# Performance work log

Measured on AMD Instinct MI355X. Metric: run time of the kernel, lower is better.

Reference implementation:

```python
import jax, jax.numpy as jnp
import numpy as np

B, S, D_IN, D_OUT = 4, 2048, 1024, 1024


def setup_inputs() -> dict:
    key = jax.random.key(0)
    ks = jax.random.split(key, 7)
    return {
        "X": jax.random.normal(ks[0], (B, S, D_IN), dtype=jnp.float32),
        "Wq": jax.random.normal(ks[1], (D_IN, D_OUT), dtype=jnp.float32) * (1.0 / np.sqrt(D_IN)),
        "bq": jax.random.normal(ks[2], (D_OUT,), dtype=jnp.float32) * 0.02,
        "Wk": jax.random.normal(ks[3], (D_IN, D_OUT), dtype=jnp.float32) * (1.0 / np.sqrt(D_IN)),
        "bk": jax.random.normal(ks[4], (D_OUT,), dtype=jnp.float32) * 0.02,
        "Wv": jax.random.normal(ks[5], (D_IN, D_OUT), dtype=jnp.float32) * (1.0 / np.sqrt(D_IN)),
        "bv": jax.random.normal(ks[6], (D_OUT,), dtype=jnp.float32) * 0.02,
    }


def reference(X, Wq, bq, Wk, bk, Wv, bv):
    # Linear projections (torch Linear: x @ W^T + b; here W stored as [in,out])
    Q = X @ Wq + bq  # [B,S,D]
    K = X @ Wk + bk
    V = X @ Wv + bv
    dk = jnp.sqrt(jnp.asarray(D_OUT, dtype=X.dtype))
    # Raw scores, lower-triangular ZEROING (not -inf), scale, softmax over keys.
    S_ = jnp.einsum('bqd,bkd->bqk', Q, K)
    S_ = jnp.tril(S_) / dk
    A = jax.nn.softmax(S_, axis=2)  # [B,S,S]
    # Faithful to torch.einsum('ijk,ijl->ijl', A, V): reduces A over k, scales V.
    out = jnp.einsum('bqk,bql->bql', A, V)
    return out
```

## Files before the change

kernel.cpp:

```cpp
#include <hip/hip_runtime.h>
#include <hip/hip_bf16.h>

#define DIN  1024
#define DOUT 1024
#define MROWS 8192

#define BM 256
#define BN 128
#define BK 64
#define NKT (DIN / BK)

typedef __attribute__((ext_vector_type(8))) short short8;
typedef __attribute__((ext_vector_type(4))) float f32x4;

__device__ __forceinline__ ushort f2bf(float f) {
    union { float f; unsigned u; } x; x.f = f;
    unsigned u = x.u + 0x7fffu + ((x.u >> 16) & 1u);
    return (ushort)(u >> 16);
}

__global__ void prep_kernel(const float* __restrict__ X, ushort* __restrict__ Xb,
                            const float* __restrict__ W, ushort* __restrict__ Wt) {
    __shared__ float tile[32][33];
    const int b = blockIdx.x;
    if (b < 2048) {
        const float4* X4 = (const float4*)X;
        ushort4* O4 = (ushort4*)Xb;
        const int n4 = MROWS * DIN / 4;
        for (int idx = b * 256 + threadIdx.x; idx < n4; idx += 2048 * 256) {
            float4 v = X4[idx];
            ushort4 o;
            o.x = f2bf(v.x); o.y = f2bf(v.y); o.z = f2bf(v.z); o.w = f2bf(v.w);
            O4[idx] = o;
        }
    } else {
        const int t = b - 2048;
        const int bx = (t & 31) * 32;
        const int by = (t >> 5) * 32;
        const int tx = threadIdx.x & 31;
        const int ty = threadIdx.x >> 5;
#pragma unroll
        for (int i = 0; i < 32; i += 8)
            tile[ty + i][tx] = W[(size_t)(by + ty + i) * DOUT + (bx + tx)];
        __syncthreads();
#pragma unroll
        for (int i = 0; i < 32; i += 8)
            Wt[(size_t)(bx + ty + i) * DIN + (by + tx)] = f2bf(tile[tx][ty + i]);
    }
}

__global__ __launch_bounds__(512, 2) void gemm_bias(
    const ushort* __restrict__ Xb,
    const ushort* __restrict__ Wt,
    const float* __restrict__ bias,
    float* __restrict__ out)
{
    __shared__ ushort As[3][BM * BK];
    __shared__ ushort Bs[3][BN * BK];

    const int tid  = threadIdx.x;
    const int lane = tid & 63;
    const int wid  = tid >> 6;
    const int wr   = wid >> 1;
    const int wc   = wid & 1;

    const int bid = blockIdx.x;
    const int swz = (bid & 7) * 32 + (bid >> 3);
    const int bm = (swz >> 3) * BM;
    const int bn = (swz & 7) * BN;

    auto stageHalf = [&](int b, int kt, int h) {
#pragma unroll
        for (int j = 0; j < 2; ++j) {
            const int c   = j * 512 + tid;
            const int rl  = c >> 3;
            const int scc = (c & 7) ^ (rl & 7);
            __builtin_amdgcn_global_load_lds(
                (const __attribute__((address_space(1))) void*)(Xb + (size_t)(bm + h * 128 + rl) * DIN + kt * BK + scc * 8),
                (__attribute__((address_space(3))) void*)(&As[b][h * 8192 + (j * 512 + wid * 64) * 8]),
                16, 0, 0);
        }
        {
            const int c   = tid;
            const int rl  = c >> 3;
            const int scc = (c & 7) ^ (rl & 7);
            __builtin_amdgcn_global_load_lds(
                (const __attribute__((address_space(1))) void*)(Wt + (size_t)(bn + h * 64 + rl) * DIN + kt * BK + scc * 8),
                (__attribute__((address_space(3))) void*)(&Bs[b][h * 4096 + wid * 512]),
                16, 0, 0);
        }
    };

    f32x4 acc[4][4];
#pragma unroll
    for (int i = 0; i < 4; ++i)
#pragma unroll
        for (int j = 0; j < 4; ++j)
            acc[i][j] = (f32x4){0.f, 0.f, 0.f, 0.f};

    auto tileBody = [&](int buf, bool doStage, int sbuf, int skt, int wait, bool bar) {
        if (doStage) {
            stageHalf(sbuf, skt, 0);
            stageHalf(sbuf, skt, 1);
        }
        short8 af[2][4], bfr[2][4];
#pragma unroll
        for (int ks = 0; ks < 2; ++ks) {
            const int sc = ((ks * 4 + (lane >> 4)) ^ (lane & 7)) * 8;
            const int am = wr * 64 + (lane & 15);
            const int bnr = wc * 64 + (lane & 15);
#pragma unroll
            for (int i = 0; i < 4; ++i)
                af[ks][i] = *(const short8*)(&As[buf][(am + i * 16) * 64 + sc]);
#pragma unroll
            for (int j = 0; j < 4; ++j)
                bfr[ks][j] = *(const short8*)(&Bs[buf][(bnr + j * 16) * 64 + sc]);
        }
        __builtin_amdgcn_s_setprio(1);
#pragma unroll
        for (int ks = 0; ks < 2; ++ks)
#pragma unroll
            for (int i = 0; i < 4; ++i)
#pragma unroll
                for (int j = 0; j < 4; ++j)
                    acc[i][j] = __builtin_amdgcn_mfma_f32_16x16x32_bf16(af[ks][i], bfr[ks][j], acc[i][j], 0, 0, 0);
        __builtin_amdgcn_s_setprio(0);
        if (wait == 2)      asm volatile("s_waitcnt vmcnt(6) lgkmcnt(0)" ::: "memory");
        else if (wait == 1) asm volatile("s_waitcnt vmcnt(0) lgkmcnt(0)" ::: "memory");
        else                asm volatile("s_waitcnt lgkmcnt(0)" ::: "memory");
        __builtin_amdgcn_sched_barrier(0);
        if (bar) __builtin_amdgcn_s_barrier();
    };

    stageHalf(0, 0, 0);
    stageHalf(0, 0, 1);
    stageHalf(1, 1, 0);
    stageHalf(1, 1, 1);
    asm volatile("s_waitcnt vmcnt(6)" ::: "memory");
    __builtin_amdgcn_sched_barrier(0);
    __builtin_amdgcn_s_barrier();

    for (int t = 0; t < NKT - 2; ++t)
        tileBody(t % 3, true, (t + 2) % 3, t + 2, 2, true);
    tileBody((NKT - 2) % 3, false, 0, 0, 1, true);
    tileBody((NKT - 1) % 3, false, 0, 0, 0, false);

    const int crow = bm + wr * 64 + (lane >> 4) * 4;
    const int ccol = bn + wc * 64 + (lane & 15);
#pragma unroll
    for (int j = 0; j < 4; ++j) {
        const int col = ccol + j * 16;
        const float bval = bias[col];
#pragma unroll
        for (int i = 0; i < 4; ++i) {
#pragma unroll
            for (int r = 0; r < 4; ++r)
                out[(size_t)(crow + i * 16 + r) * DOUT + col] = acc[i][j][r] + bval;
        }
    }
}

__global__ void gemm_naive(const float* __restrict__ X, const float* __restrict__ W,
                           const float* __restrict__ b, float* __restrict__ out) {
    int n = blockIdx.x * blockDim.x + threadIdx.x;
    int m = blockIdx.y;
    float acc = b[n];
    for (int k = 0; k < DIN; ++k)
        acc += X[(size_t)m * DIN + k] * W[(size_t)k * DOUT + n];
    out[(size_t)m * DOUT + n] = acc;
}

extern "C" void kernel_launch(void* const* d_in, const int* in_sizes, int n_in,
                              void* d_out, int out_size, void* d_ws, size_t ws_size,
                              hipStream_t stream) {
    const float* X  = (const float*)d_in[0];
    const float* Wv = (const float*)d_in[5];
    const float* bv = (const float*)d_in[6];
    float* out = (float*)d_out;

    const size_t xb_elems = (size_t)MROWS * DIN;
    const size_t wt_elems = (size_t)DOUT * DIN;
    const size_t needed = (xb_elems + wt_elems) * sizeof(ushort);

    if (ws_size < needed) {
        dim3 g(DOUT / 256, MROWS);
        gemm_naive<<<g, 256, 0, stream>>>(X, Wv, bv, out);
        return;
    }

    ushort* Xb = (ushort*)d_ws;
    ushort* Wt = Xb + xb_elems;

    prep_kernel<<<2048 + 1024, 256, 0, stream>>>(X, Xb, Wv, Wt);
    gemm_bias<<<256, 512, 0, stream>>>(Xb, Wt, bv, out);
}
```

Before: 40.62 us.

## Fuse fp32-to-bf16 conversion of X into GEMM via register-staged A tiles

Drops the separate pass that converts X to bf16 into a workspace. The GEMM now loads fp32 X rows into registers, converts them and writes swizzled bf16 into LDS, while W^T still arrives by direct global-to-LDS DMA. This removes a full write and re-read of the bf16 copy of X. In exchange, the pipeline shrinks from a triple-buffered, partially waited schedule to a double buffer with a full vmcnt(0) wait every k-step, register pressure rises, and each block reads twice as many bytes of X.

```diff
diff --git a/kernel.cpp b/kernel.cpp
--- a/kernel.cpp
+++ b/kernel.cpp
@@ -19,44 +19,30 @@
     return (ushort)(u >> 16);
 }
 
-__global__ void prep_kernel(const float* __restrict__ X, ushort* __restrict__ Xb,
-                            const float* __restrict__ W, ushort* __restrict__ Wt) {
+__global__ void prep_wt(const float* __restrict__ W, ushort* __restrict__ Wt) {
     __shared__ float tile[32][33];
-    const int b = blockIdx.x;
-    if (b < 2048) {
-        const float4* X4 = (const float4*)X;
-        ushort4* O4 = (ushort4*)Xb;
-        const int n4 = MROWS * DIN / 4;
-        for (int idx = b * 256 + threadIdx.x; idx < n4; idx += 2048 * 256) {
-            float4 v = X4[idx];
-            ushort4 o;
-            o.x = f2bf(v.x); o.y = f2bf(v.y); o.z = f2bf(v.z); o.w = f2bf(v.w);
-            O4[idx] = o;
-        }
-    } else {
-        const int t = b - 2048;
-        const int bx = (t & 31) * 32;
-        const int by = (t >> 5) * 32;
-        const int tx = threadIdx.x & 31;
-        const int ty = threadIdx.x >> 5;
+    const int t  = blockIdx.x;
+    const int bx = (t & 31) * 32;
+    const int by = (t >> 5) * 32;
+    const int tx = threadIdx.x & 31;
+    const int ty = threadIdx.x >> 5;
 #pragma unroll
-        for (int i = 0; i < 32; i += 8)
-            tile[ty + i][tx] = W[(size_t)(by + ty + i) * DOUT + (bx + tx)];
-        __syncthreads();
+    for (int i = 0; i < 32; i += 8)
+        tile[ty + i][tx] = W[(size_t)(by + ty + i) * DOUT + (bx + tx)];
+    __syncthreads();
 #pragma unroll
-        for (int i = 0; i < 32; i += 8)
-            Wt[(size_t)(bx + ty + i) * DIN + (by + tx)] = f2bf(tile[tx][ty + i]);
-    }
+    for (int i = 0; i < 32; i += 8)
+        Wt[(size_t)(bx + ty + i) * DIN + (by + tx)] = f2bf(tile[tx][ty + i]);
 }
 
-__global__ __launch_bounds__(512, 2) void gemm_bias(
-    const ushort* __restrict__ Xb,
+__global__ __launch_bounds__(512, 2) void gemm_fused(
+    const float*  __restrict__ X,
     const ushort* __restrict__ Wt,
-    const float* __restrict__ bias,
+    const float*  __restrict__ bias,
     float* __restrict__ out)
 {
-    __shared__ ushort As[3][BM * BK];
-    __shared__ ushort Bs[3][BN * BK];
+    __shared__ ushort As[2][BM * BK];
+    __shared__ ushort Bs[2][BN * BK];
 
     const int tid  = threadIdx.x;
     const int lane = tid & 63;
@@ -69,24 +55,38 @@
     const int bm = (swz >> 3) * BM;
     const int bn = (swz & 7) * BN;
 
-    auto stageHalf = [&](int b, int kt, int h) {
+    const int ar_ = tid >> 1;
+    const int ah_ = tid & 1;
+    const float* aSrc = X + (size_t)(bm + ar_) * DIN + ah_ * 32;
+
+    float4 areg[8];
+    auto loadA = [&](int kt) {
+        const float4* p = (const float4*)(aSrc + kt * BK);
+#pragma unroll
+        for (int i = 0; i < 8; ++i) areg[i] = p[i];
+    };
+    auto writeA = [&](int b) {
+        ushort* row = &As[b][ar_ * BK];
+#pragma unroll
+        for (int w = 0; w < 4; ++w) {
+            const float4 a0 = areg[w * 2], a1 = areg[w * 2 + 1];
+            short8 v;
+            v[0] = f2bf(a0.x); v[1] = f2bf(a0.y); v[2] = f2bf(a0.z); v[3] = f2bf(a0.w);
+            v[4] = f2bf(a1.x); v[5] = f2bf(a1.y); v[6] = f2bf(a1.z); v[7] = f2bf(a1.w);
+            const int slot = (ah_ * 4 + w) ^ (ar_ & 7);
+            *(short8*)(row + slot * 8) = v;
+        }
+    };
+
+    auto dmaB = [&](int b, int kt) {
 #pragma unroll
         for (int j = 0; j < 2; ++j) {
-            const int c   = j * 512 + tid;
-            const int rl  = c >> 3;
-            const int scc = (c & 7) ^ (rl & 7);
+            const int c  = j * 512 + tid;
+            const int rl = c >> 3;
+            const int sl = (c & 7) ^ (rl & 7);
             __builtin_amdgcn_global_load_lds(
-                (const __attribute__((address_space(1))) void*)(Xb + (size_t)(bm + h * 128 + rl) * DIN + kt * BK + scc * 8),
-                (__attribute__((address_space(3))) void*)(&As[b][h * 8192 + (j * 512 + wid * 64) * 8]),
-                16, 0, 0);
-        }
-        {
-            const int c   = tid;
-            const int rl  = c >> 3;
-            const int scc = (c & 7) ^ (rl & 7);
-            __builtin_amdgcn_global_load_lds(
-                (const __attribute__((address_space(1))) void*)(Wt + (size_t)(bn + h * 64 + rl) * DIN + kt * BK + scc * 8),
-                (__attribute__((address_space(3))) void*)(&Bs[b][h * 4096 + wid * 512]),
+                (const __attribute__((address_space(1))) void*)(Wt + (size_t)(bn + rl) * DIN + kt * BK + sl * 8),
+                (__attribute__((address_space(3))) void*)(&Bs[b][(j * 512 + wid * 64) * 8]),
                 16, 0, 0);
         }
     };
@@ -98,24 +98,18 @@
         for (int j = 0; j < 4; ++j)
             acc[i][j] = (f32x4){0.f, 0.f, 0.f, 0.f};
 
-    auto tileBody = [&](int buf, bool doStage, int sbuf, int skt, int wait, bool bar) {
-        if (doStage) {
-            stageHalf(sbuf, skt, 0);
-            stageHalf(sbuf, skt, 1);
-        }
-        short8 af[2][4], bfr[2][4];
+    const int am  = wr * 64 + (lane & 15);
+    const int bnr = wc * 64 + (lane & 15);
+    auto fragRead = [&](int b, int ks, short8* af, short8* bfr) {
+        const int sc = ((ks * 4 + (lane >> 4)) ^ (lane & 7)) * 8;
 #pragma unroll
-        for (int ks = 0; ks < 2; ++ks) {
-            const int sc = ((ks * 4 + (lane >> 4)) ^ (lane & 7)) * 8;
-            const int am = wr * 64 + (lane & 15);
-            const int bnr = wc * 64 + (lane & 15);
+        for (int i = 0; i < 4; ++i)
+            af[i] = *(const short8*)(&As[b][(am + i * 16) * BK + sc]);
 #pragma unroll
-            for (int i = 0; i < 4; ++i)
-                af[ks][i] = *(const short8*)(&As[buf][(am + i * 16) * 64 + sc]);
-#pragma unroll
-            for (int j = 0; j < 4; ++j)
-                bfr[ks][j] = *(const short8*)(&Bs[buf][(bnr + j * 16) * 64 + sc]);
-        }
+        for (int j = 0; j < 4; ++j)
+            bfr[j] = *(const short8*)(&Bs[b][(bnr + j * 16) * BK + sc]);
+    };
+    auto mfmaCluster = [&](short8 af[2][4], short8 bfr[2][4]) {
         __builtin_amdgcn_s_setprio(1);
 #pragma unroll
         for (int ks = 0; ks < 2; ++ks)
@@ -125,25 +119,35 @@
                 for (int j = 0; j < 4; ++j)
                     acc[i][j] = __builtin_amdgcn_mfma_f32_16x16x32_bf16(af[ks][i], bfr[ks][j], acc[i][j], 0, 0, 0);
         __builtin_amdgcn_s_setprio(0);
-        if (wait == 2)      asm volatile("s_waitcnt vmcnt(6) lgkmcnt(0)" ::: "memory");
-        else if (wait == 1) asm volatile("s_waitcnt vmcnt(0) lgkmcnt(0)" ::: "memory");
-        else                asm volatile("s_waitcnt lgkmcnt(0)" ::: "memory");
-        __builtin_amdgcn_sched_barrier(0);
-        if (bar) __builtin_amdgcn_s_barrier();
     };
 
-    stageHalf(0, 0, 0);
-    stageHalf(0, 0, 1);
-    stageHalf(1, 1, 0);
-    stageHalf(1, 1, 1);
-    asm volatile("s_waitcnt vmcnt(6)" ::: "memory");
-    __builtin_amdgcn_sched_barrier(0);
+    loadA(0);
+    dmaB(0, 0);
+    writeA(0);
+    asm volatile("s_waitcnt vmcnt(0) lgkmcnt(0)" ::: "memory");
     __builtin_amdgcn_s_barrier();
 
-    for (int t = 0; t < NKT - 2; ++t)
-        tileBody(t % 3, true, (t + 2) % 3, t + 2, 2, true);
-    tileBody((NKT - 2) % 3, false, 0, 0, 1, true);
-    tileBody((NKT - 1) % 3, false, 0, 0, 0, false);
+    int buf = 0;
+    for (int t = 0; t < NKT - 1; ++t) {
+        loadA(t + 1);
+        dmaB(buf ^ 1, t + 1);
+        __builtin_amdgcn_sched_barrier(0);
+        short8 af[2][4], bfr[2][4];
+        fragRead(buf, 0, af[0], bfr[0]);
+        fragRead(buf, 1, af[1], bfr[1]);
+        mfmaCluster(af, bfr);
+        writeA(buf ^ 1);
+        asm volatile("s_waitcnt vmcnt(0) lgkmcnt(0)" ::: "memory");
+        __builtin_amdgcn_sched_barrier(0);
+        __builtin_amdgcn_s_barrier();
+        buf ^= 1;
+    }
+    {
+        short8 af[2][4], bfr[2][4];
+        fragRead(buf, 0, af[0], bfr[0]);
+        fragRead(buf, 1, af[1], bfr[1]);
+        mfmaCluster(af, bfr);
+    }
 
     const int crow = bm + wr * 64 + (lane >> 4) * 4;
     const int ccol = bn + wc * 64 + (lane & 15);
@@ -178,19 +182,14 @@
     const float* bv = (const float*)d_in[6];
     float* out = (float*)d_out;
 
-    const size_t xb_elems = (size_t)MROWS * DIN;
     const size_t wt_elems = (size_t)DOUT * DIN;
-    const size_t needed = (xb_elems + wt_elems) * sizeof(ushort);
-
-    if (ws_size < needed) {
+    if (ws_size < wt_elems * sizeof(ushort)) {
         dim3 g(DOUT / 256, MROWS);
         gemm_naive<<<g, 256, 0, stream>>>(X, Wv, bv, out);
         return;
     }
 
-    ushort* Xb = (ushort*)d_ws;
-    ushort* Wt = Xb + xb_elems;
-
-    prep_kernel<<<2048 + 1024, 256, 0, stream>>>(X, Xb, Wv, Wt);
-    gemm_bias<<<256, 512, 0, stream>>>(Xb, Wt, bv, out);
+    ushort* Wt = (ushort*)d_ws;
+    prep_wt<<<1024, 256, 0, stream>>>(Wv, Wt);
+    gemm_fused<<<256, 512, 0, stream>>>(X, Wt, bv, out);
 }
```

After: 62.26 us. 53.3% more time.

## Load B fragments directly from global into registers, split tile into two phases

Applied to the files above, without the earlier changes.

Removes the LDS staging buffer for the weight tile and instead has each wave load its B fragments straight from global memory into registers, double-buffered one k-tile ahead. The main loop is split into two half-k phases with a barrier and staging of A interleaved per phase, with new vmcnt thresholds. This cuts LDS traffic and capacity for B, possibly raising occupancy, but adds redundant global loads of B across waves sharing a column, more register pressure, and more barriers per tile.

```diff
diff --git a/kernel.cpp b/kernel.cpp
--- a/kernel.cpp
+++ b/kernel.cpp
@@ -56,7 +56,6 @@
     float* __restrict__ out)
 {
     __shared__ ushort As[3][BM * BK];
-    __shared__ ushort Bs[3][BN * BK];
 
     const int tid  = threadIdx.x;
     const int lane = tid & 63;
@@ -69,7 +68,7 @@
     const int bm = (swz >> 3) * BM;
     const int bn = (swz & 7) * BN;
 
-    auto stageHalf = [&](int b, int kt, int h) {
+    auto stageA = [&](int b, int kt, int h) {
 #pragma unroll
         for (int j = 0; j < 2; ++j) {
             const int c   = j * 512 + tid;
@@ -80,15 +79,15 @@
                 (__attribute__((address_space(3))) void*)(&As[b][h * 8192 + (j * 512 + wid * 64) * 8]),
                 16, 0, 0);
         }
-        {
-            const int c   = tid;
-            const int rl  = c >> 3;
-            const int scc = (c & 7) ^ (rl & 7);
-            __builtin_amdgcn_global_load_lds(
-                (const __attribute__((address_space(1))) void*)(Wt + (size_t)(bn + h * 64 + rl) * DIN + kt * BK + scc * 8),
-                (__attribute__((address_space(3))) void*)(&Bs[b][h * 4096 + wid * 512]),
-                16, 0, 0);
-        }
+    };
+
+    const ushort* bBase = Wt + (size_t)(bn + wc * 64 + (lane & 15)) * DIN + (lane >> 4) * 8;
+    auto loadB = [&](short8 (&dst)[2][4], int kt) {
+#pragma unroll
+        for (int ks = 0; ks < 2; ++ks)
+#pragma unroll
+            for (int j = 0; j < 4; ++j)
+                dst[ks][j] = *(const short8*)(bBase + (size_t)j * 16 * DIN + kt * BK + ks * 32);
     };
 
     f32x4 acc[4][4];
@@ -98,52 +97,62 @@
         for (int j = 0; j < 4; ++j)
             acc[i][j] = (f32x4){0.f, 0.f, 0.f, 0.f};
 
-    auto tileBody = [&](int buf, bool doStage, int sbuf, int skt, int wait, bool bar) {
-        if (doStage) {
-            stageHalf(sbuf, skt, 0);
-            stageHalf(sbuf, skt, 1);
-        }
-        short8 af[2][4], bfr[2][4];
-#pragma unroll
-        for (int ks = 0; ks < 2; ++ks) {
-            const int sc = ((ks * 4 + (lane >> 4)) ^ (lane & 7)) * 8;
-            const int am = wr * 64 + (lane & 15);
-            const int bnr = wc * 64 + (lane & 15);
+    const int am = wr * 64 + (lane & 15);
+
+    auto phase = [&](int buf, int ks, const short8 (&bcur)[2][4],
+                     bool doStage, int sbuf, int skt, int wait, bool endBar) {
+        short8 af[4];
+        const int sc = ((ks * 4 + (lane >> 4)) ^ (lane & 7)) * 8;
+#pragma unroll
+        for (int i = 0; i < 4; ++i)
+            af[i] = *(const short8*)(&As[buf][(am + i * 16) * BK + sc]);
+        if (doStage) stageA(sbuf, skt, ks);
+        __builtin_amdgcn_s_barrier();
+        asm volatile("s_waitcnt lgkmcnt(0)" ::: "memory");
+        __builtin_amdgcn_sched_barrier(0);
+        __builtin_amdgcn_s_setprio(1);
+        if (ks == 0) {
 #pragma unroll
             for (int i = 0; i < 4; ++i)
-                af[ks][i] = *(const short8*)(&As[buf][(am + i * 16) * 64 + sc]);
-#pragma unroll
-            for (int j = 0; j < 4; ++j)
-                bfr[ks][j] = *(const short8*)(&Bs[buf][(bnr + j * 16) * 64 + sc]);
-        }
-        __builtin_amdgcn_s_setprio(1);
-#pragma unroll
-        for (int ks = 0; ks < 2; ++ks)
+#pragma unroll
+                for (int j = 0; j < 4; ++j)
+                    acc[i][j] = __builtin_amdgcn_mfma_f32_16x16x32_bf16(af[i], bcur[0][j], acc[i][j], 0, 0, 0);
+        } else {
 #pragma unroll
             for (int i = 0; i < 4; ++i)
 #pragma unroll
                 for (int j = 0; j < 4; ++j)
-                    acc[i][j] = __builtin_amdgcn_mfma_f32_16x16x32_bf16(af[ks][i], bfr[ks][j], acc[i][j], 0, 0, 0);
+                    acc[i][j] = __builtin_amdgcn_mfma_f32_16x16x32_bf16(af[i], bcur[1][j], acc[i][j], 0, 0, 0);
+        }
         __builtin_amdgcn_s_setprio(0);
-        if (wait == 2)      asm volatile("s_waitcnt vmcnt(6) lgkmcnt(0)" ::: "memory");
-        else if (wait == 1) asm volatile("s_waitcnt vmcnt(0) lgkmcnt(0)" ::: "memory");
-        else                asm volatile("s_waitcnt lgkmcnt(0)" ::: "memory");
-        __builtin_amdgcn_sched_barrier(0);
-        if (bar) __builtin_amdgcn_s_barrier();
-    };
-
-    stageHalf(0, 0, 0);
-    stageHalf(0, 0, 1);
-    stageHalf(1, 1, 0);
-    stageHalf(1, 1, 1);
-    asm volatile("s_waitcnt vmcnt(6)" ::: "memory");
-    __builtin_amdgcn_sched_barrier(0);
+        if (wait == 12)     asm volatile("s_waitcnt vmcnt(12)" ::: "memory");
+        else if (wait == 8) asm volatile("s_waitcnt vmcnt(8)"  ::: "memory");
+        else if (wait == 0) asm volatile("s_waitcnt vmcnt(0)"  ::: "memory");
+        if (endBar) __builtin_amdgcn_s_barrier();
+    };
+
+    short8 bA[2][4], bB[2][4];
+
+    stageA(0, 0, 0); stageA(0, 0, 1);
+    loadB(bA, 0);
+    stageA(1, 1, 0); stageA(1, 1, 1);
+    asm volatile("s_waitcnt vmcnt(12)" ::: "memory");
     __builtin_amdgcn_s_barrier();
 
-    for (int t = 0; t < NKT - 2; ++t)
-        tileBody(t % 3, true, (t + 2) % 3, t + 2, 2, true);
-    tileBody((NKT - 2) % 3, false, 0, 0, 1, true);
-    tileBody((NKT - 1) % 3, false, 0, 0, 0, false);
+    auto tileBody = [&](int t, const short8 (&cur)[2][4], short8 (&nxt)[2][4],
+                        bool doLoadB, bool doStage, int wait, bool last) {
+        const int buf = t % 3;
+        if (doLoadB) loadB(nxt, t + 1);
+        phase(buf, 0, cur, doStage, (t + 2) % 3, t + 2, -1, true);
+        phase(buf, 1, cur, doStage, (t + 2) % 3, t + 2, wait, !last);
+    };
+
+    for (int tt = 0; tt < NKT - 2; tt += 2) {
+        tileBody(tt,     bA, bB, true, true, 12, false);
+        tileBody(tt + 1, bB, bA, true, true, 12, false);
+    }
+    tileBody(NKT - 2, bA, bB, true,  false, 8, false);
+    tileBody(NKT - 1, bB, bA, false, false, -1, true);
 
     const int crow = bm + wr * 64 + (lane >> 4) * 4;
     const int ccol = bn + wc * 64 + (lane & 15);
```

After: 59.43 us. +46.3%, slower.

## Shrink GEMM tile to 128x128 with simple double-buffered pipeline

Applied to the files above, without the earlier changes.

Halves the M tile to 128 rows, uses 256-thread blocks and 512 workgroups, and replaces the triple-buffered pipeline (explicit waitcnt, setprio, sched barriers) with a plain double-buffered loop synced by __syncthreads. The goal is more workgroups across the CUs and lower LDS use per block. In exchange, B-tile reuse per block drops and the hand-tuned overlap of loads and MFMA is lost.

```diff
diff --git a/kernel.cpp b/kernel.cpp
--- a/kernel.cpp
+++ b/kernel.cpp
@@ -5,7 +5,7 @@
 #define DOUT 1024
 #define MROWS 8192
 
-#define BM 256
+#define BM 128
 #define BN 128
 #define BK 64
 #define NKT (DIN / BK)
@@ -49,14 +49,14 @@
     }
 }
 
-__global__ __launch_bounds__(512, 2) void gemm_bias(
+__global__ __launch_bounds__(256, 2) void gemm_bias(
     const ushort* __restrict__ Xb,
     const ushort* __restrict__ Wt,
     const float* __restrict__ bias,
     float* __restrict__ out)
 {
-    __shared__ ushort As[3][BM * BK];
-    __shared__ ushort Bs[3][BN * BK];
+    __shared__ ushort As[2][BM * BK];
+    __shared__ ushort Bs[2][BN * BK];
 
     const int tid  = threadIdx.x;
     const int lane = tid & 63;
@@ -65,28 +65,29 @@
     const int wc   = wid & 1;
 
     const int bid = blockIdx.x;
-    const int swz = (bid & 7) * 32 + (bid >> 3);
+    const int swz = (bid & 7) * 64 + (bid >> 3);
     const int bm = (swz >> 3) * BM;
     const int bn = (swz & 7) * BN;
 
-    auto stageHalf = [&](int b, int kt, int h) {
+    auto stage = [&](int b, int kt) {
 #pragma unroll
-        for (int j = 0; j < 2; ++j) {
-            const int c   = j * 512 + tid;
+        for (int i = 0; i < 4; ++i) {
+            const int c   = i * 256 + tid;
             const int rl  = c >> 3;
             const int scc = (c & 7) ^ (rl & 7);
             __builtin_amdgcn_global_load_lds(
-                (const __attribute__((address_space(1))) void*)(Xb + (size_t)(bm + h * 128 + rl) * DIN + kt * BK + scc * 8),
-                (__attribute__((address_space(3))) void*)(&As[b][h * 8192 + (j * 512 + wid * 64) * 8]),
+                (const __attribute__((address_space(1))) void*)(Xb + (size_t)(bm + rl) * DIN + kt * BK + scc * 8),
+                (__attribute__((address_space(3))) void*)(&As[b][(i * 256 + wid * 64) * 8]),
                 16, 0, 0);
         }
-        {
-            const int c   = tid;
+#pragma unroll
+        for (int i = 0; i < 4; ++i) {
+            const int c   = i * 256 + tid;
             const int rl  = c >> 3;
             const int scc = (c & 7) ^ (rl & 7);
             __builtin_amdgcn_global_load_lds(
-                (const __attribute__((address_space(1))) void*)(Wt + (size_t)(bn + h * 64 + rl) * DIN + kt * BK + scc * 8),
-                (__attribute__((address_space(3))) void*)(&Bs[b][h * 4096 + wid * 512]),
+                (const __attribute__((address_space(1))) void*)(Wt + (size_t)(bn + rl) * DIN + kt * BK + scc * 8),
+                (__attribute__((address_space(3))) void*)(&Bs[b][(i * 256 + wid * 64) * 8]),
                 16, 0, 0);
         }
     };
@@ -98,52 +99,33 @@
         for (int j = 0; j < 4; ++j)
             acc[i][j] = (f32x4){0.f, 0.f, 0.f, 0.f};
 
-    auto tileBody = [&](int buf, bool doStage, int sbuf, int skt, int wait, bool bar) {
-        if (doStage) {
-            stageHalf(sbuf, skt, 0);
-            stageHalf(sbuf, skt, 1);
-        }
-        short8 af[2][4], bfr[2][4];
+    const int am  = wr * 64 + (lane & 15);
+    const int bnr = wc * 64 + (lane & 15);
+
+    stage(0, 0);
+    __syncthreads();
+
+    for (int t = 0; t < NKT; ++t) {
+        const int buf = t & 1;
+        if (t < NKT - 1) stage(buf ^ 1, t + 1);
 #pragma unroll
         for (int ks = 0; ks < 2; ++ks) {
+            short8 af[4], bfr[4];
             const int sc = ((ks * 4 + (lane >> 4)) ^ (lane & 7)) * 8;
-            const int am = wr * 64 + (lane & 15);
-            const int bnr = wc * 64 + (lane & 15);
 #pragma unroll
             for (int i = 0; i < 4; ++i)
-                af[ks][i] = *(const short8*)(&As[buf][(am + i * 16) * 64 + sc]);
+                af[i] = *(const short8*)(&As[buf][(am + i * 16) * BK + sc]);
 #pragma unroll
             for (int j = 0; j < 4; ++j)
-                bfr[ks][j] = *(const short8*)(&Bs[buf][(bnr + j * 16) * 64 + sc]);
-        }
-        __builtin_amdgcn_s_setprio(1);
-#pragma unroll
-        for (int ks = 0; ks < 2; ++ks)
+                bfr[j] = *(const short8*)(&Bs[buf][(bnr + j * 16) * BK + sc]);
 #pragma unroll
             for (int i = 0; i < 4; ++i)
 #pragma unroll
                 for (int j = 0; j < 4; ++j)
-                    acc[i][j] = __builtin_amdgcn_mfma_f32_16x16x32_bf16(af[ks][i], bfr[ks][j], acc[i][j], 0, 0, 0);
-        __builtin_amdgcn_s_setprio(0);
-        if (wait == 2)      asm volatile("s_waitcnt vmcnt(6) lgkmcnt(0)" ::: "memory");
-        else if (wait == 1) asm volatile("s_waitcnt vmcnt(0) lgkmcnt(0)" ::: "memory");
-        else                asm volatile("s_waitcnt lgkmcnt(0)" ::: "memory");
-        __builtin_amdgcn_sched_barrier(0);
-        if (bar) __builtin_amdgcn_s_barrier();
-    };
-
-    stageHalf(0, 0, 0);
-    stageHalf(0, 0, 1);
-    stageHalf(1, 1, 0);
-    stageHalf(1, 1, 1);
-    asm volatile("s_waitcnt vmcnt(6)" ::: "memory");
-    __builtin_amdgcn_sched_barrier(0);
-    __builtin_amdgcn_s_barrier();
-
-    for (int t = 0; t < NKT - 2; ++t)
-        tileBody(t % 3, true, (t + 2) % 3, t + 2, 2, true);
-    tileBody((NKT - 2) % 3, false, 0, 0, 1, true);
-    tileBody((NKT - 1) % 3, false, 0, 0, 0, false);
+                    acc[i][j] = __builtin_amdgcn_mfma_f32_16x16x32_bf16(af[i], bfr[j], acc[i][j], 0, 0, 0);
+        }
+        __syncthreads();
+    }
 
     const int crow = bm + wr * 64 + (lane >> 4) * 4;
     const int ccol = bn + wc * 64 + (lane & 15);
@@ -192,5 +174,5 @@
     ushort* Wt = Xb + xb_elems;
 
     prep_kernel<<<2048 + 1024, 256, 0, stream>>>(X, Xb, Wv, Wt);
-    gemm_bias<<<256, 512, 0, stream>>>(Xb, Wt, bv, out);
+    gemm_bias<<<512, 256, 0, stream>>>(Xb, Wt, bv, out);
 }
```

Result: no change. 41.23 us (+1.5%).
